# Kernel tuning notes

Hardware: AMD Instinct MI355X
Metric: run time of the kernel (lower is better)

The kernel has to match this reference:

```python
import jax, jax.numpy as jnp
import numpy as np
import math

B, T, C, H = 4, 2048, 1024, 4
D = C // H
SCALE = 1.0 / math.sqrt(D)
EPS = 1e-5

def _cln(x, w, b):
    # channel-first LayerNorm over C of (B, C, T)
    mu = jnp.mean(x, axis=1, keepdims=True)
    r = x - mu
    s = jnp.mean(r * r, axis=1, keepdims=True)
    return r / jnp.sqrt(s + EPS) * w + b

def _dwconv(x, w, b=None):
    # depthwise conv1d: x (B, C, T), w (C, 1, 3), stride 1, pad 1
    y = jax.lax.conv_general_dilated(x, w, (1,), [(1, 1)], dimension_numbers=('NCH', 'OIH', 'NCH'), feature_group_count=x.shape[1])
    if b is not None:
        y = y + b[None, :, None]
    return y

def _conv1x1(x, w, b):
    # pointwise conv: x (B, C, T), w (Cout, Cin), b (Cout,)
    return jnp.einsum('oc,bct->bot', w, x) + b[None, :, None]

def _forward(x, mask, norm1_w, norm1_b, qconv_w, kconv_w, vconv_w, qnorm_w, qnorm_b, knorm_w, knorm_b, vnorm_w, vnorm_b, q1_w, q1_b, k1_w, k1_b, v1_w, v1_b, proj_w, proj_b, norm2_w, norm2_b, lin1_w, lin1_b, tc_w, tc_b, lin2_w, lin2_b):
    xc = jnp.swapaxes(x, 1, 2)                      # (B, C, T)
    h = _cln(xc, norm1_w, norm1_b)
    mf = mask.astype(x.dtype)                       # (B, 1, T); stride 1 -> interpolate is identity
    q = _conv1x1(_cln(_dwconv(h, qconv_w) * mf, qnorm_w, qnorm_b), q1_w, q1_b)
    k = _conv1x1(_cln(_dwconv(h, kconv_w) * mf, knorm_w, knorm_b), k1_w, k1_b)
    v = _conv1x1(_cln(_dwconv(h, vconv_w) * mf, vnorm_w, vnorm_b), v1_w, v1_b)
    # (B, H, T, D)
    q = jnp.swapaxes(q.reshape(B, H, D, T), 2, 3)
    k = jnp.swapaxes(k.reshape(B, H, D, T), 2, 3)
    v = jnp.swapaxes(v.reshape(B, H, D, T), 2, 3)
    att = jnp.einsum('bhqd,bhkd->bhqk', q * SCALE, k)
    att = jnp.where(mask[:, :, None, :], att, -jnp.inf)
    att = jax.nn.softmax(att, axis=-1)
    out = jnp.einsum('bhqk,bhkd->bhqd', att, v * mf[:, :, :, None])
    out = jnp.swapaxes(out, 2, 3).reshape(B, C, T)
    out = _conv1x1(out, proj_w, proj_b) * mf        # qx_mask == mask for stride 1
    x = x + jnp.swapaxes(out, 1, 2)                 # residual, (B, T, C)
    # Local_cnn branch
    h2 = jnp.swapaxes(_cln(jnp.swapaxes(x, 1, 2), norm2_w, norm2_b), 1, 2)  # (B, T, C)
    y = h2 @ lin1_w.T + lin1_b
    y = jnp.swapaxes(_dwconv(jnp.swapaxes(y, 1, 2), tc_w, tc_b), 1, 2)
    y = jax.nn.gelu(y, approximate=False)
    y = y @ lin2_w.T + lin2_b
    return x + y

def setup_inputs():
    key = jax.random.key(0)
    ks = jax.random.split(key, 16)
    f32 = jnp.float32
    x = jax.random.normal(ks[0], (B, T, C), dtype=f32)
    lengths = jax.random.randint(ks[1], (B,), T // 2, T + 1)
    mask = jnp.arange(T)[None, None, :] < lengths[:, None, None]  # (B, 1, T) bool
    dw_std = math.sqrt(2.0 / 3.0)
    px_std = math.sqrt(2.0 / C)
    d = dict(x=x, mask=mask)
    d['norm1_w'] = jnp.ones((1, C, 1), f32); d['norm1_b'] = jnp.zeros((1, C, 1), f32)
    d['qconv_w'] = jax.random.normal(ks[2], (C, 1, 3), dtype=f32) * dw_std
    d['kconv_w'] = jax.random.normal(ks[3], (C, 1, 3), dtype=f32) * dw_std
    d['vconv_w'] = jax.random.normal(ks[4], (C, 1, 3), dtype=f32) * dw_std
    for nm in ['qnorm', 'knorm', 'vnorm']:
        d[nm + '_w'] = jnp.ones((1, C, 1), f32); d[nm + '_b'] = jnp.zeros((1, C, 1), f32)
    d['q1_w'] = jax.random.normal(ks[5], (C, C), dtype=f32) * px_std; d['q1_b'] = jnp.zeros((C,), f32)
    d['k1_w'] = jax.random.normal(ks[6], (C, C), dtype=f32) * px_std; d['k1_b'] = jnp.zeros((C,), f32)
    d['v1_w'] = jax.random.normal(ks[7], (C, C), dtype=f32) * px_std; d['v1_b'] = jnp.zeros((C,), f32)
    d['proj_w'] = jax.random.normal(ks[8], (C, C), dtype=f32) * px_std; d['proj_b'] = jnp.zeros((C,), f32)
    d['norm2_w'] = jnp.ones((1, C, 1), f32); d['norm2_b'] = jnp.zeros((1, C, 1), f32)
    d['lin1_w'] = jax.random.normal(ks[9], (C, C), dtype=f32) * 0.02; d['lin1_b'] = jnp.zeros((C,), f32)
    d['tc_w'] = jax.random.normal(ks[10], (C, 1, 3), dtype=f32) * dw_std; d['tc_b'] = jnp.zeros((C,), f32)
    d['lin2_w'] = jax.random.normal(ks[11], (C, C), dtype=f32) * 0.02; d['lin2_b'] = jnp.zeros((C,), f32)
    return d

def reference(x, mask, norm1_w, norm1_b, qconv_w, kconv_w, vconv_w, qnorm_w, qnorm_b, knorm_w, knorm_b, vnorm_w, vnorm_b, q1_w, q1_b, k1_w, k1_b, v1_w, v1_b, proj_w, proj_b, norm2_w, norm2_b, lin1_w, lin1_b, tc_w, tc_b, lin2_w, lin2_b):
    return _forward(x, mask, norm1_w, norm1_b, qconv_w, kconv_w, vconv_w, qnorm_w, qnorm_b, knorm_w, knorm_b, vnorm_w, vnorm_b, q1_w, q1_b, k1_w, k1_b, v1_w, v1_b, proj_w, proj_b, norm2_w, norm2_b, lin1_w, lin1_b, tc_w, tc_b, lin2_w, lin2_b)
```

## Files before the change

kernel.cpp:

```cpp
#include <hip/hip_runtime.h>

#define BB 4
#define TT 2048
#define CC 1024
#define HH 4
#define DD 256
#define MM (BB*TT)

#define EPSV 1e-5f
#define NEGBIG (-1e30f)
#define SCALEV 0.0625f

typedef unsigned short u16;
typedef unsigned int   u32;
typedef __bf16 bf16x8 __attribute__((ext_vector_type(8)));
typedef float  f32x4  __attribute__((ext_vector_type(4)));
typedef float  f32x16 __attribute__((ext_vector_type(16)));

typedef u32 __attribute__((address_space(1))) gu32;
typedef u32 __attribute__((address_space(3))) lu32;

__device__ __forceinline__ u16 f2bf(float f){
  u32 u = __builtin_bit_cast(u32, f);
  u32 r = (u + 0x7fffu + ((u >> 16) & 1u)) >> 16;
  return (u16)r;
}
__device__ __forceinline__ float bf2f(u16 h){
  u32 u = ((u32)h) << 16;
  return __builtin_bit_cast(float, u);
}
__device__ __forceinline__ void gload_lds16(const u16* g, u16* l){
  __builtin_amdgcn_global_load_lds((const gu32*)g, (lu32*)l, 16, 0, 0);
}
__device__ __forceinline__ u32 cvtpk_bf16(float lo, float hi){
  u32 r;
  asm("v_cvt_pk_bf16_f32 %0, %1, %2" : "=v"(r) : "v"(lo), "v"(hi));
  return r;
}

__global__ __launch_bounds__(256) void conv_w_kernel(
    const float* __restrict__ w0, const float* __restrict__ w1, const float* __restrict__ w2,
    const float* __restrict__ w3, const float* __restrict__ w4, const float* __restrict__ w5,
    u16* __restrict__ o0, u16* __restrict__ o1, u16* __restrict__ o2,
    u16* __restrict__ o3, u16* __restrict__ o4, u16* __restrict__ o5){
  const int i = (blockIdx.x * 256 + threadIdx.x) * 4;
  const float* wsrc[6] = {w0,w1,w2,w3,w4,w5};
  u16* odst[6] = {o0,o1,o2,o3,o4,o5};
#pragma unroll
  for (int k = 0; k < 6; ++k){
    float4 v = *(const float4*)(wsrc[k] + i);
    ushort4 p; p.x=f2bf(v.x); p.y=f2bf(v.y); p.z=f2bf(v.z); p.w=f2bf(v.w);
    *(ushort4*)(odst[k] + i) = p;
  }
}

template<int OUTBF>
__global__ __launch_bounds__(256) void ln_rows(const float* __restrict__ x,
    const float* __restrict__ g, const float* __restrict__ be, void* __restrict__ out){
  const int row = blockIdx.x, tid = threadIdx.x;
  const float4 v = ((const float4*)(x + (size_t)row * CC))[tid];
  float s  = v.x + v.y + v.z + v.w;
  float ss = v.x*v.x + v.y*v.y + v.z*v.z + v.w*v.w;
  __shared__ float sb[8];
#pragma unroll
  for (int o = 1; o < 64; o <<= 1){ s += __shfl_xor(s, o); ss += __shfl_xor(ss, o); }
  const int wid = tid >> 6, lane = tid & 63;
  if (lane == 0){ sb[wid] = s; sb[4 + wid] = ss; }
  __syncthreads();
  s  = sb[0] + sb[1] + sb[2] + sb[3];
  ss = sb[4] + sb[5] + sb[6] + sb[7];
  const float mu = s * (1.0f / CC);
  const float rstd = rsqrtf(ss * (1.0f / CC) - mu * mu + EPSV);
  const float4 gg = ((const float4*)g)[tid];
  const float4 bb = ((const float4*)be)[tid];
  const float r0 = (v.x - mu) * rstd * gg.x + bb.x;
  const float r1 = (v.y - mu) * rstd * gg.y + bb.y;
  const float r2 = (v.z - mu) * rstd * gg.z + bb.z;
  const float r3 = (v.w - mu) * rstd * gg.w + bb.w;
  if (OUTBF){
    ushort4 p; p.x=f2bf(r0); p.y=f2bf(r1); p.z=f2bf(r2); p.w=f2bf(r3);
    *(ushort4*)((u16*)out + (size_t)row * CC + tid * 4) = p;
  } else {
    ((float4*)((float*)out + (size_t)row * CC))[tid] = make_float4(r0, r1, r2, r3);
  }
}

__global__ __launch_bounds__(256) void qkv_pre(const float* __restrict__ h,
    const int* __restrict__ mask,
    const float* __restrict__ qw, const float* __restrict__ kw, const float* __restrict__ vw,
    const float* __restrict__ qg, const float* __restrict__ qb2,
    const float* __restrict__ kg, const float* __restrict__ kb2,
    const float* __restrict__ vg, const float* __restrict__ vb2,
    u16* __restrict__ qn, u16* __restrict__ kn, u16* __restrict__ vn){
  const int row = blockIdx.x, tid = threadIdx.x;
  const int t = row & (TT - 1);
  const float mf = mask[row] ? 1.f : 0.f;
  const float4 z4 = make_float4(0.f, 0.f, 0.f, 0.f);
  const float4 x0 = ((const float4*)(h + (size_t)row * CC))[tid];
  const float4 xm = (t > 0)      ? ((const float4*)(h + (size_t)(row - 1) * CC))[tid] : z4;
  const float4 xp = (t < TT - 1) ? ((const float4*)(h + (size_t)(row + 1) * CC))[tid] : z4;
  const int c = tid * 4;
  const float am[4] = {xm.x, xm.y, xm.z, xm.w};
  const float a0[4] = {x0.x, x0.y, x0.z, x0.w};
  const float ap[4] = {xp.x, xp.y, xp.z, xp.w};
  float yq[4], yk[4], yv[4];
  float sq=0.f, ssq=0.f, sk=0.f, ssk=0.f, sv=0.f, ssv=0.f;
#pragma unroll
  for (int i = 0; i < 4; ++i){
    const float* qwp = qw + (c + i) * 3;
    const float* kwp = kw + (c + i) * 3;
    const float* vwp = vw + (c + i) * 3;
    const float q_ = (am[i]*qwp[0] + a0[i]*qwp[1] + ap[i]*qwp[2]) * mf;
    const float k_ = (am[i]*kwp[0] + a0[i]*kwp[1] + ap[i]*kwp[2]) * mf;
    const float v_ = (am[i]*vwp[0] + a0[i]*vwp[1] + ap[i]*vwp[2]) * mf;
    yq[i]=q_; yk[i]=k_; yv[i]=v_;
    sq+=q_; ssq+=q_*q_; sk+=k_; ssk+=k_*k_; sv+=v_; ssv+=v_*v_;
  }
  __shared__ float sb[24];
#pragma unroll
  for (int o = 1; o < 64; o <<= 1){
    sq += __shfl_xor(sq, o); ssq += __shfl_xor(ssq, o);
    sk += __shfl_xor(sk, o); ssk += __shfl_xor(ssk, o);
    sv += __shfl_xor(sv, o); ssv += __shfl_xor(ssv, o);
  }
  const int wid = tid >> 6, lane = tid & 63;
  if (lane == 0){
    sb[wid]=sq; sb[4+wid]=ssq; sb[8+wid]=sk; sb[12+wid]=ssk; sb[16+wid]=sv; sb[20+wid]=ssv;
  }
  __syncthreads();
  sq  = sb[0]+sb[1]+sb[2]+sb[3];    ssq = sb[4]+sb[5]+sb[6]+sb[7];
  sk  = sb[8]+sb[9]+sb[10]+sb[11];  ssk = sb[12]+sb[13]+sb[14]+sb[15];
  sv  = sb[16]+sb[17]+sb[18]+sb[19];ssv = sb[20]+sb[21]+sb[22]+sb[23];
  {
    const float mu = sq * (1.f/CC), rstd = rsqrtf(ssq*(1.f/CC) - mu*mu + EPSV);
    ushort4 p;
    p.x = f2bf((yq[0]-mu)*rstd*qg[c+0] + qb2[c+0]);
    p.y = f2bf((yq[1]-mu)*rstd*qg[c+1] + qb2[c+1]);
    p.z = f2bf((yq[2]-mu)*rstd*qg[c+2] + qb2[c+2]);
    p.w = f2bf((yq[3]-mu)*rstd*qg[c+3] + qb2[c+3]);
    *(ushort4*)(qn + (size_t)row * CC + c) = p;
  }
  {
    const float mu = sk * (1.f/CC), rstd = rsqrtf(ssk*(1.f/CC) - mu*mu + EPSV);
    ushort4 p;
    p.x = f2bf((yk[0]-mu)*rstd*kg[c+0] + kb2[c+0]);
    p.y = f2bf((yk[1]-mu)*rstd*kg[c+1] + kb2[c+1]);
    p.z = f2bf((yk[2]-mu)*rstd*kg[c+2] + kb2[c+2]);
    p.w = f2bf((yk[3]-mu)*rstd*kg[c+3] + kb2[c+3]);
    *(ushort4*)(kn + (size_t)row * CC + c) = p;
  }
  {
    const float mu = sv * (1.f/CC), rstd = rsqrtf(ssv*(1.f/CC) - mu*mu + EPSV);
    ushort4 p;
    p.x = f2bf((yv[0]-mu)*rstd*vg[c+0] + vb2[c+0]);
    p.y = f2bf((yv[1]-mu)*rstd*vg[c+1] + vb2[c+1]);
    p.z = f2bf((yv[2]-mu)*rstd*vg[c+2] + vb2[c+2]);
    p.w = f2bf((yv[3]-mu)*rstd*vg[c+3] + vb2[c+3]);
    *(ushort4*)(vn + (size_t)row * CC + c) = p;
  }
}

__device__ __forceinline__ void gemm_core(const u16* __restrict__ A, const u16* __restrict__ Bw,
    u16* As, u16* Bs, f32x4 acc[4][4], int bm, int bn, int tid){
  const int lane = tid & 63, wid = tid >> 6;
  const int wr = wid >> 1, wc = wid & 1;
  const int la = lane & 15, lg = lane >> 4;
  const int srow = tid >> 3;
  const int schunk = (tid & 7) ^ (srow & 7);
  const u16* gA = A  + (size_t)(bm * 128 + srow) * CC + schunk * 8;
  const u16* gB = Bw + (size_t)(bn * 128 + srow) * CC + schunk * 8;
  u16* dA = As + tid * 8;
  u16* dB = Bs + tid * 8;
  const int swz = (la & 7) << 4;
  for (int kt = 0; kt < CC / 64; ++kt){
#pragma unroll
    for (int i = 0; i < 4; ++i){
      gload_lds16(gA + (size_t)(i * 32) * CC + kt * 64, dA + i * 2048);
      gload_lds16(gB + (size_t)(i * 32) * CC + kt * 64, dB + i * 2048);
    }
    __syncthreads();
#pragma unroll
    for (int kk = 0; kk < 2; ++kk){
      bf16x8 af[4], bf[4];
      const int co = (kk * 64 + lg * 16) ^ swz;
#pragma unroll
      for (int mi = 0; mi < 4; ++mi)
        af[mi] = *(const bf16x8*)((const char*)As + (wr * 64 + mi * 16 + la) * 128 + co);
#pragma unroll
      for (int ni = 0; ni < 4; ++ni)
        bf[ni] = *(const bf16x8*)((const char*)Bs + (wc * 64 + ni * 16 + la) * 128 + co);
#pragma unroll
      for (int mi = 0; mi < 4; ++mi)
#pragma unroll
        for (int ni = 0; ni < 4; ++ni)
          acc[mi][ni] = __builtin_amdgcn_mfma_f32_16x16x32_bf16(af[mi], bf[ni], acc[mi][ni], 0, 0, 0);
    }
    __syncthreads();
  }
}

template<int MODE>
__global__ __launch_bounds__(256) void gemm_bt(
    const u16* __restrict__ A, const u16* __restrict__ Bw,
    const float* __restrict__ bias, void* __restrict__ out,
    const float* __restrict__ resid, const int* __restrict__ mask){
  __shared__ __align__(16) u16 As[128 * 64];
  __shared__ __align__(16) u16 Bs[128 * 64];
  const int tid = threadIdx.x, lane = tid & 63, wid = tid >> 6;
  const int wr = wid >> 1, wc = wid & 1;
  const int bm = blockIdx.x, bn = blockIdx.y;
  f32x4 acc[4][4];
#pragma unroll
  for (int i = 0; i < 4; ++i)
#pragma unroll
    for (int j = 0; j < 4; ++j) acc[i][j] = (f32x4){0.f, 0.f, 0.f, 0.f};
  gemm_core(A, Bw, As, Bs, acc, bm, bn, tid);
  const int la = lane & 15, lg = lane >> 4;
#pragma unroll
  for (int mi = 0; mi < 4; ++mi){
    const int mb = bm * 128 + wr * 64 + mi * 16 + lg * 4;
#pragma unroll
    for (int ni = 0; ni < 4; ++ni){
      const int n = bn * 128 + wc * 64 + ni * 16 + la;
      const float bz = bias[n];
      if (MODE == 0){
        u16* o = (u16*)out;
#pragma unroll
        for (int j = 0; j < 4; ++j) o[(size_t)(mb + j) * CC + n] = f2bf(acc[mi][ni][j] + bz);
      } else if (MODE == 1){
        float* o = (float*)out;
#pragma unroll
        for (int j = 0; j < 4; ++j){
          const int m = mb + j;
          const float mf = mask[m] ? 1.f : 0.f;
          o[(size_t)m * CC + n] = (acc[mi][ni][j] + bz) * mf + resid[(size_t)m * CC + n];
        }
      } else {
        float* o = (float*)out;
#pragma unroll
        for (int j = 0; j < 4; ++j){
          const int m = mb + j;
          o[(size_t)m * CC + n] = acc[mi][ni][j] + bz + resid[(size_t)m * CC + n];
        }
      }
    }
  }
}

__global__ __launch_bounds__(256) void gemm_qkv(
    const u16* __restrict__ qn, const u16* __restrict__ kn, const u16* __restrict__ vn,
    const u16* __restrict__ wq, const u16* __restrict__ wk, const u16* __restrict__ wv,
    const float* __restrict__ qb, const float* __restrict__ kb, const float* __restrict__ vb,
    u16* __restrict__ Qb, u16* __restrict__ Kb, u16* __restrict__ Vtb){
  __shared__ __align__(16) u16 As[128 * 64];
  __shared__ __align__(16) u16 Bs[128 * 64];
  const int z = blockIdx.z;
  const u16* A  = (z == 0) ? qn : (z == 1) ? kn : vn;
  const u16* Bw = (z == 0) ? wq : (z == 1) ? wk : wv;
  const float* bias = (z == 0) ? qb : (z == 1) ? kb : vb;
  const int tid = threadIdx.x, lane = tid & 63, wid = tid >> 6;
  const int wr = wid >> 1, wc = wid & 1;
  const int bm = blockIdx.x, bn = blockIdx.y;
  f32x4 acc[4][4];
#pragma unroll
  for (int i = 0; i < 4; ++i)
#pragma unroll
    for (int j = 0; j < 4; ++j) acc[i][j] = (f32x4){0.f, 0.f, 0.f, 0.f};
  gemm_core(A, Bw, As, Bs, acc, bm, bn, tid);
  const int la = lane & 15, lg = lane >> 4;
#pragma unroll
  for (int mi = 0; mi < 4; ++mi){
    const int mb = bm * 128 + wr * 64 + mi * 16 + lg * 4;
#pragma unroll
    for (int ni = 0; ni < 4; ++ni){
      const int n = bn * 128 + wc * 64 + ni * 16 + la;
      const float bz = bias[n];
      if (z < 2){
        u16* o = z ? Kb : Qb;
#pragma unroll
        for (int j = 0; j < 4; ++j) o[(size_t)(mb + j) * CC + n] = f2bf(acc[mi][ni][j] + bz);
      } else {
        const int bq = mb >> 11, tq = mb & (TT - 1);
        const int hq = n >> 8, dq = n & 255;
        ushort4 p;
        p.x = f2bf(acc[mi][ni][0] + bz); p.y = f2bf(acc[mi][ni][1] + bz);
        p.z = f2bf(acc[mi][ni][2] + bz); p.w = f2bf(acc[mi][ni][3] + bz);
        *(ushort4*)&Vtb[(size_t)((bq * HH + hq) * DD + dq) * TT + tq] = p;
      }
    }
  }
}

__global__ __launch_bounds__(256, 2) void flash_attn(
    const u16* __restrict__ Q, const u16* __restrict__ Kg,
    const u16* __restrict__ Vt, const int* __restrict__ mask,
    u16* __restrict__ Os0, u16* __restrict__ Os1, float2* __restrict__ stats){
  __shared__ __align__(16) u16 Ks[32 * 256];
  __shared__ __align__(16) u16 Vs[256 * 32];
  const int Dn = blockIdx.x;
  const int xcd = Dn & 7, rest = Dn >> 3;
  const int bh = xcd * 2 + (rest >> 5);
  const int sub = rest & 31;
  const int qt = sub >> 1, sp = sub & 1;
  const int b = bh >> 2, h2 = bh & 3;
  const int tid = threadIdx.x, lane = tid & 63, wid = tid >> 6;
  const int l31 = lane & 31, hi = lane >> 5;

  const int* mrow = mask + b * TT;
  int len = 1024;
  {
    unsigned long long bal = __ballot(mrow[1024 + lane * 16] != 0);
    int ones = __popcll(bal);
    if (ones > 0){
      int lo = 1024 + (ones - 1) * 16;
      unsigned long long bal2 = __ballot(mrow[lo + (lane & 15)] != 0);
      len = lo + __popcll(bal2 & 0xFFFFull);
    }
  }
  const int nkt = (len + 31) >> 5;
  const int hk = (nkt + 1) >> 1;
  const int t0 = sp ? hk : 0, t1 = sp ? nkt : hk;

  const int q0 = qt * 128 + wid * 32;
  bf16x8 qf[16];
  const u16* qrow = Q + (size_t)(b * TT + q0 + l31) * CC + h2 * DD + hi * 8;
#pragma unroll
  for (int kd = 0; kd < 16; ++kd) qf[kd] = *(const bf16x8*)(qrow + kd * 16);

  f32x16 acc[8];
#pragma unroll
  for (int i = 0; i < 8; ++i)
#pragma unroll
    for (int r = 0; r < 16; ++r) acc[i][r] = 0.f;
  float mrun = NEGBIG, lrun = 0.f;

  const int krow = tid >> 5;
  const int kc = (tid & 31) ^ (krow & 7);
  const u16* ksrc = Kg + (size_t)(b * TT + krow) * CC + h2 * DD + kc * 8;
  const int vc = (tid & 3) ^ ((tid >> 3) & 3);
  const u16* vsrcb = Vt + (size_t)(bh * DD + (tid >> 2)) * TT + vc * 8;

#define STAGE_K(KT) { _Pragma("unroll") \
  for (int i = 0; i < 4; ++i) \
    gload_lds16(ksrc + (size_t)((KT) * 32 + i * 8) * CC, Ks + i * 2048 + tid * 8); }
#define STAGE_V(KT) { _Pragma("unroll") \
  for (int i = 0; i < 4; ++i) \
    gload_lds16(vsrcb + (size_t)(i * 64) * TT + (KT) * 32, Vs + i * 2048 + tid * 8); }

  STAGE_K(t0); STAGE_V(t0);
  __syncthreads();

  const char* KsB = (const char*)Ks;
  const char* VsB = (const char*)Vs;
  const int swk = (l31 & 7) << 4;
  const int swv = ((l31 >> 1) & 3) << 4;
  const float sc2 = SCALEV * 1.44269504f;

  for (int kt = t0; kt < t1; ++kt){
    f32x16 s;
#pragma unroll
    for (int r = 0; r < 16; ++r) s[r] = 0.f;
#pragma unroll
    for (int kd = 0; kd < 16; ++kd){
      bf16x8 kf = *(const bf16x8*)(KsB + l31 * 512 + ((kd * 32 + hi * 16) ^ swk));
      s = __builtin_amdgcn_mfma_f32_32x32x16_bf16(kf, qf[kd], s, 0, 0, 0);
    }
    if (kt * 32 + 32 <= len){
      s *= sc2;
    } else {
#pragma unroll
      for (int r = 0; r < 16; ++r){
        const int k = kt * 32 + (r & 3) + 8 * (r >> 2) + 4 * hi;
        s[r] = (k < len) ? s[r] * sc2 : NEGBIG;
      }
    }
    float tm = s[0];
#pragma unroll
    for (int r = 1; r < 16; ++r) tm = fmaxf(tm, s[r]);
    tm = fmaxf(tm, __shfl_xor(tm, 32));
    if (!__all(tm <= mrun + 12.0f)){
      const float mn = fmaxf(mrun, tm);
      const float al = __builtin_exp2f(mrun - mn);
      mrun = mn; lrun *= al;
#pragma unroll
      for (int i = 0; i < 8; ++i) acc[i] *= al;
    }
    float p[16];
    float ts = 0.f;
#pragma unroll
    for (int r = 0; r < 16; ++r){ p[r] = __builtin_exp2f(s[r] - mrun); ts += p[r]; }
    ts += __shfl_xor(ts, 32);
    lrun += ts;
    u32 w0 = cvtpk_bf16(p[0],  p[1]),  w1 = cvtpk_bf16(p[2],  p[3]);
    u32 w2 = cvtpk_bf16(p[4],  p[5]),  w3 = cvtpk_bf16(p[6],  p[7]);
    u32 w4 = cvtpk_bf16(p[8],  p[9]),  w5 = cvtpk_bf16(p[10], p[11]);
    u32 w6 = cvtpk_bf16(p[12], p[13]), w7 = cvtpk_bf16(p[14], p[15]);
    asm("v_permlane32_swap_b32 %0, %1" : "+v"(w0), "+v"(w2));
    asm("v_permlane32_swap_b32 %0, %1" : "+v"(w1), "+v"(w3));
    asm("v_permlane32_swap_b32 %0, %1" : "+v"(w4), "+v"(w6));
    asm("v_permlane32_swap_b32 %0, %1" : "+v"(w5), "+v"(w7));
    u32 pb0u[4] = {w0, w1, w2, w3};
    u32 pb1u[4] = {w4, w5, w6, w7};
    bf16x8 pb0 = __builtin_bit_cast(bf16x8, *(uint4*)pb0u);
    bf16x8 pb1 = __builtin_bit_cast(bf16x8, *(uint4*)pb1u);
    __syncthreads();
    if (kt + 1 < t1) STAGE_K(kt + 1);
#pragma unroll
    for (int dt = 0; dt < 8; ++dt){
      const char* vr = VsB + (dt * 32 + l31) * 64;
      bf16x8 vf0 = *(const bf16x8*)(vr + ((hi * 16) ^ swv));
      acc[dt] = __builtin_amdgcn_mfma_f32_32x32x16_bf16(vf0, pb0, acc[dt], 0, 0, 0);
      bf16x8 vf1 = *(const bf16x8*)(vr + ((32 + hi * 16) ^ swv));
      acc[dt] = __builtin_amdgcn_mfma_f32_32x32x16_bf16(vf1, pb1, acc[dt], 0, 0, 0);
    }
    __syncthreads();
    if (kt + 1 < t1) STAGE_V(kt + 1);
  }
  u16* Os = sp ? Os1 : Os0;
  u16* orow = Os + (size_t)(b * TT + q0 + l31) * CC + h2 * DD + hi * 4;
#pragma unroll
  for (int dt = 0; dt < 8; ++dt)
#pragma unroll
    for (int rg = 0; rg < 4; ++rg){
      ushort4 pk;
      pk.x = f2bf(acc[dt][rg * 4 + 0]); pk.y = f2bf(acc[dt][rg * 4 + 1]);
      pk.z = f2bf(acc[dt][rg * 4 + 2]); pk.w = f2bf(acc[dt][rg * 4 + 3]);
      *(ushort4*)(orow + dt * 32 + rg * 8) = pk;
    }
  if (lane < 32)
    stats[(size_t)((sp * 16 + bh) << 11) + q0 + l31] = make_float2(mrun, lrun);
#undef STAGE_K
#undef STAGE_V
}

__global__ __launch_bounds__(256) void attn_combine(
    const u16* __restrict__ Os0, const u16* __restrict__ Os1,
    const float2* __restrict__ stats, u16* __restrict__ AO){
  const int row = blockIdx.x, tid = threadIdx.x;
  const int b = row >> 11, q = row & (TT - 1);
  const int h2 = tid >> 6;
  const int bh = b * HH + h2;
  const float2 sA = stats[(size_t)(bh << 11) + q];
  const float2 sB = stats[(size_t)((16 + bh) << 11) + q];
  const float m = fmaxf(sA.x, sB.x);
  const float eA = __builtin_exp2f(sA.x - m), eB = __builtin_exp2f(sB.x - m);
  const float l = sA.y * eA + sB.y * eB;
  const float fA = eA / l, fB = eB / l;
  const size_t off = (size_t)row * CC + tid * 4;
  const ushort4 a = *(const ushort4*)(Os0 + off);
  const ushort4 c = *(const ushort4*)(Os1 + off);
  ushort4 o;
  o.x = f2bf(bf2f(a.x) * fA + bf2f(c.x) * fB);
  o.y = f2bf(bf2f(a.y) * fA + bf2f(c.y) * fB);
  o.z = f2bf(bf2f(a.z) * fA + bf2f(c.z) * fB);
  o.w = f2bf(bf2f(a.w) * fA + bf2f(c.w) * fB);
  *(ushort4*)(AO + off) = o;
}

__global__ __launch_bounds__(256) void tc_gelu(const u16* __restrict__ y2,
    const float* __restrict__ w, const float* __restrict__ bias, u16* __restrict__ y3){
  const int row = blockIdx.x, tid = threadIdx.x;
  const int t = row & (TT - 1);
  const int c = tid * 4;
  ushort4 z4; z4.x = z4.y = z4.z = z4.w = 0;
  const ushort4 u0 = *(const ushort4*)(y2 + (size_t)row * CC + c);
  const ushort4 um = (t > 0)      ? *(const ushort4*)(y2 + (size_t)(row - 1) * CC + c) : z4;
  const ushort4 up = (t < TT - 1) ? *(const ushort4*)(y2 + (size_t)(row + 1) * CC + c) : z4;
  const float am[4] = {bf2f(um.x), bf2f(um.y), bf2f(um.z), bf2f(um.w)};
  const float a0[4] = {bf2f(u0.x), bf2f(u0.y), bf2f(u0.z), bf2f(u0.w)};
  const float ap[4] = {bf2f(up.x), bf2f(up.y), bf2f(up.z), bf2f(up.w)};
  u16 pv[4];
#pragma unroll
  for (int i = 0; i < 4; ++i){
    const float* wp = w + (c + i) * 3;
    const float yv = am[i] * wp[0] + a0[i] * wp[1] + ap[i] * wp[2] + bias[c + i];
    const float ge = 0.5f * yv * (1.f + erff(yv * 0.7071067811865475f));
    pv[i] = f2bf(ge);
  }
  ushort4 p; p.x = pv[0]; p.y = pv[1]; p.z = pv[2]; p.w = pv[3];
  *(ushort4*)(y3 + (size_t)row * CC + c) = p;
}

extern "C" void kernel_launch(void* const* d_in, const int* in_sizes, int n_in,
                              void* d_out, int out_size, void* d_ws, size_t ws_size,
                              hipStream_t stream){
  const float* x     = (const float*)d_in[0];
  const int*   mask  = (const int*)d_in[1];
  const float* n1g   = (const float*)d_in[2];
  const float* n1b   = (const float*)d_in[3];
  const float* qconv = (const float*)d_in[4];
  const float* kconv = (const float*)d_in[5];
  const float* vconv = (const float*)d_in[6];
  const float* qg    = (const float*)d_in[7];
  const float* qbe   = (const float*)d_in[8];
  const float* kg    = (const float*)d_in[9];
  const float* kbe   = (const float*)d_in[10];
  const float* vg    = (const float*)d_in[11];
  const float* vbe   = (const float*)d_in[12];
  const float* q1w   = (const float*)d_in[13];
  const float* q1b   = (const float*)d_in[14];
  const float* k1w   = (const float*)d_in[15];
  const float* k1b   = (const float*)d_in[16];
  const float* v1w   = (const float*)d_in[17];
  const float* v1b   = (const float*)d_in[18];
  const float* pw    = (const float*)d_in[19];
  const float* pb    = (const float*)d_in[20];
  const float* n2g   = (const float*)d_in[21];
  const float* n2b   = (const float*)d_in[22];
  const float* l1w   = (const float*)d_in[23];
  const float* l1b   = (const float*)d_in[24];
  const float* tcw   = (const float*)d_in[25];
  const float* tcb   = (const float*)d_in[26];
  const float* l2w   = (const float*)d_in[27];
  const float* l2b   = (const float*)d_in[28];
  (void)in_sizes; (void)n_in; (void)out_size; (void)ws_size;

  char* ws = (char*)d_ws;
  const size_t MB = (size_t)1 << 20;
  u16* wq  = (u16*)(ws + 0 * MB);
  u16* wk  = (u16*)(ws + 2 * MB);
  u16* wv  = (u16*)(ws + 4 * MB);
  u16* wp2 = (u16*)(ws + 6 * MB);
  u16* wl1 = (u16*)(ws + 8 * MB);
  u16* wl2 = (u16*)(ws + 10 * MB);
  float* hbuf = (float*)(ws + 12 * MB);
  float* x2   = hbuf;
  u16* qn  = (u16*)(ws + 44 * MB);
  u16* kn  = (u16*)(ws + 60 * MB);
  u16* vn  = (u16*)(ws + 76 * MB);
  u16* Qb  = (u16*)(ws + 92 * MB);
  u16* Kb  = (u16*)(ws + 108 * MB);
  u16* Vtb = (u16*)(ws + 124 * MB);
  float2* stats = (float2*)(ws + 140 * MB);
  u16* AO  = qn;
  u16* Os0 = kn;
  u16* Os1 = vn;
  u16* y1  = kn;
  u16* y2  = vn;
  u16* y3  = Qb;

  conv_w_kernel<<<1024, 256, 0, stream>>>(q1w, k1w, v1w, pw, l1w, l2w, wq, wk, wv, wp2, wl1, wl2);
  ln_rows<0><<<MM, 256, 0, stream>>>(x, n1g, n1b, hbuf);
  qkv_pre<<<MM, 256, 0, stream>>>(hbuf, mask, qconv, kconv, vconv,
                                  qg, qbe, kg, kbe, vg, vbe, qn, kn, vn);
  gemm_qkv<<<dim3(64, 8, 3), 256, 0, stream>>>(qn, kn, vn, wq, wk, wv, q1b, k1b, v1b, Qb, Kb, Vtb);
  flash_attn<<<512, 256, 0, stream>>>(Qb, Kb, Vtb, mask, Os0, Os1, stats);
  attn_combine<<<MM, 256, 0, stream>>>(Os0, Os1, stats, AO);
  gemm_bt<1><<<dim3(64, 8), 256, 0, stream>>>(AO, wp2, pb, x2, x, mask);
  ln_rows<1><<<MM, 256, 0, stream>>>(x2, n2g, n2b, y1);
  gemm_bt<0><<<dim3(64, 8), 256, 0, stream>>>(y1, wl1, l1b, y2, nullptr, nullptr);
  tc_gelu<<<MM, 256, 0, stream>>>(y2, tcw, tcb, y3);
  gemm_bt<2><<<dim3(64, 8), 256, 0, stream>>>(y3, wl2, l2b, (float*)d_out, x2, nullptr);
}
```

Baseline: 340.4 us.

## Store LN1 output in bf16, halve flash-attn block size, raise GEMM occupancy hints

The first LayerNorm now writes bf16 instead of fp32, so the depthwise-conv/QKV pre-kernel reads half the bytes. Flash attention moves from 256-thread blocks covering 128 queries to 128-thread blocks covering 64 queries, doubling the grid to 1024 blocks, with K/V staging loops and index remapping adjusted to match. The GEMM kernels gain a min-blocks-per-CU hint of 3 to push more waves per CU, at the risk of register spills. The bf16 LN output adds rounding error ahead of the conv and norm stages.

```diff
diff --git a/kernel.cpp b/kernel.cpp
--- a/kernel.cpp
+++ b/kernel.cpp
@@ -85,7 +85,7 @@
   }
 }
 
-__global__ __launch_bounds__(256) void qkv_pre(const float* __restrict__ h,
+__global__ __launch_bounds__(256) void qkv_pre(const u16* __restrict__ h,
     const int* __restrict__ mask,
     const float* __restrict__ qw, const float* __restrict__ kw, const float* __restrict__ vw,
     const float* __restrict__ qg, const float* __restrict__ qb2,
@@ -95,14 +95,14 @@
   const int row = blockIdx.x, tid = threadIdx.x;
   const int t = row & (TT - 1);
   const float mf = mask[row] ? 1.f : 0.f;
-  const float4 z4 = make_float4(0.f, 0.f, 0.f, 0.f);
-  const float4 x0 = ((const float4*)(h + (size_t)row * CC))[tid];
-  const float4 xm = (t > 0)      ? ((const float4*)(h + (size_t)(row - 1) * CC))[tid] : z4;
-  const float4 xp = (t < TT - 1) ? ((const float4*)(h + (size_t)(row + 1) * CC))[tid] : z4;
+  ushort4 z4; z4.x = z4.y = z4.z = z4.w = 0;
+  const ushort4 x0 = ((const ushort4*)(h + (size_t)row * CC))[tid];
+  const ushort4 xm = (t > 0)      ? ((const ushort4*)(h + (size_t)(row - 1) * CC))[tid] : z4;
+  const ushort4 xp = (t < TT - 1) ? ((const ushort4*)(h + (size_t)(row + 1) * CC))[tid] : z4;
   const int c = tid * 4;
-  const float am[4] = {xm.x, xm.y, xm.z, xm.w};
-  const float a0[4] = {x0.x, x0.y, x0.z, x0.w};
-  const float ap[4] = {xp.x, xp.y, xp.z, xp.w};
+  const float am[4] = {bf2f(xm.x), bf2f(xm.y), bf2f(xm.z), bf2f(xm.w)};
+  const float a0[4] = {bf2f(x0.x), bf2f(x0.y), bf2f(x0.z), bf2f(x0.w)};
+  const float ap[4] = {bf2f(xp.x), bf2f(xp.y), bf2f(xp.z), bf2f(xp.w)};
   float yq[4], yk[4], yv[4];
   float sq=0.f, ssq=0.f, sk=0.f, ssk=0.f, sv=0.f, ssv=0.f;
 #pragma unroll
@@ -200,7 +200,7 @@
 }
 
 template<int MODE>
-__global__ __launch_bounds__(256) void gemm_bt(
+__global__ __launch_bounds__(256, 3) void gemm_bt(
     const u16* __restrict__ A, const u16* __restrict__ Bw,
     const float* __restrict__ bias, void* __restrict__ out,
     const float* __restrict__ resid, const int* __restrict__ mask){
@@ -247,7 +247,7 @@
   }
 }
 
-__global__ __launch_bounds__(256) void gemm_qkv(
+__global__ __launch_bounds__(256, 3) void gemm_qkv(
     const u16* __restrict__ qn, const u16* __restrict__ kn, const u16* __restrict__ vn,
     const u16* __restrict__ wq, const u16* __restrict__ wk, const u16* __restrict__ wv,
     const float* __restrict__ qb, const float* __restrict__ kb, const float* __restrict__ vb,
@@ -291,7 +291,7 @@
   }
 }
 
-__global__ __launch_bounds__(256, 2) void flash_attn(
+__global__ __launch_bounds__(128, 2) void flash_attn(
     const u16* __restrict__ Q, const u16* __restrict__ Kg,
     const u16* __restrict__ Vt, const int* __restrict__ mask,
     u16* __restrict__ Os0, u16* __restrict__ Os1, float2* __restrict__ stats){
@@ -299,8 +299,8 @@
   __shared__ __align__(16) u16 Vs[256 * 32];
   const int Dn = blockIdx.x;
   const int xcd = Dn & 7, rest = Dn >> 3;
-  const int bh = xcd * 2 + (rest >> 5);
-  const int sub = rest & 31;
+  const int bh = xcd * 2 + (rest >> 6);
+  const int sub = rest & 63;
   const int qt = sub >> 1, sp = sub & 1;
   const int b = bh >> 2, h2 = bh & 3;
   const int tid = threadIdx.x, lane = tid & 63, wid = tid >> 6;
@@ -321,7 +321,7 @@
   const int hk = (nkt + 1) >> 1;
   const int t0 = sp ? hk : 0, t1 = sp ? nkt : hk;
 
-  const int q0 = qt * 128 + wid * 32;
+  const int q0 = qt * 64 + wid * 32;
   bf16x8 qf[16];
   const u16* qrow = Q + (size_t)(b * TT + q0 + l31) * CC + h2 * DD + hi * 8;
 #pragma unroll
@@ -334,18 +334,18 @@
     for (int r = 0; r < 16; ++r) acc[i][r] = 0.f;
   float mrun = NEGBIG, lrun = 0.f;
 
-  const int krow = tid >> 5;
-  const int kc = (tid & 31) ^ (krow & 7);
-  const u16* ksrc = Kg + (size_t)(b * TT + krow) * CC + h2 * DD + kc * 8;
-  const int vc = (tid & 3) ^ ((tid >> 3) & 3);
-  const u16* vsrcb = Vt + (size_t)(bh * DD + (tid >> 2)) * TT + vc * 8;
+  const int kr0 = tid >> 5;
+  const u16* ksrcE = Kg + (size_t)(b * TT + kr0) * CC + h2 * DD + (((tid & 31) ^ kr0) * 8);
+  const u16* ksrcO = Kg + (size_t)(b * TT + kr0) * CC + h2 * DD + (((tid & 31) ^ (kr0 | 4)) * 8);
+  const u16* vsrc  = Vt + (size_t)(bh * DD + (tid >> 2)) * TT + (((tid & 3) ^ ((tid >> 3) & 3)) * 8);
 
 #define STAGE_K(KT) { _Pragma("unroll") \
-  for (int i = 0; i < 4; ++i) \
-    gload_lds16(ksrc + (size_t)((KT) * 32 + i * 8) * CC, Ks + i * 2048 + tid * 8); }
+  for (int i = 0; i < 8; ++i){ \
+    const u16* srcp = (i & 1) ? ksrcO : ksrcE; \
+    gload_lds16(srcp + (size_t)((KT) * 32 + i * 4) * CC, Ks + i * 1024 + tid * 8); } }
 #define STAGE_V(KT) { _Pragma("unroll") \
-  for (int i = 0; i < 4; ++i) \
-    gload_lds16(vsrcb + (size_t)(i * 64) * TT + (KT) * 32, Vs + i * 2048 + tid * 8); }
+  for (int i = 0; i < 8; ++i) \
+    gload_lds16(vsrc + (size_t)(i * 32) * TT + (KT) * 32, Vs + i * 1024 + tid * 8); }
 
   STAGE_K(t0); STAGE_V(t0);
   __syncthreads();
@@ -427,7 +427,7 @@
       pk.z = f2bf(acc[dt][rg * 4 + 2]); pk.w = f2bf(acc[dt][rg * 4 + 3]);
       *(ushort4*)(orow + dt * 32 + rg * 8) = pk;
     }
-  if (lane < 32)
+  if ((lane & 32) == 0)
     stats[(size_t)((sp * 16 + bh) << 11) + q0 + l31] = make_float2(mrun, lrun);
 #undef STAGE_K
 #undef STAGE_V
@@ -523,8 +523,8 @@
   u16* wp2 = (u16*)(ws + 6 * MB);
   u16* wl1 = (u16*)(ws + 8 * MB);
   u16* wl2 = (u16*)(ws + 10 * MB);
-  float* hbuf = (float*)(ws + 12 * MB);
-  float* x2   = hbuf;
+  u16* hbuf = (u16*)(ws + 12 * MB);
+  float* x2 = (float*)(ws + 12 * MB);
   u16* qn  = (u16*)(ws + 44 * MB);
   u16* kn  = (u16*)(ws + 60 * MB);
   u16* vn  = (u16*)(ws + 76 * MB);
@@ -540,11 +540,11 @@
   u16* y3  = Qb;
 
   conv_w_kernel<<<1024, 256, 0, stream>>>(q1w, k1w, v1w, pw, l1w, l2w, wq, wk, wv, wp2, wl1, wl2);
-  ln_rows<0><<<MM, 256, 0, stream>>>(x, n1g, n1b, hbuf);
+  ln_rows<1><<<MM, 256, 0, stream>>>(x, n1g, n1b, hbuf);
   qkv_pre<<<MM, 256, 0, stream>>>(hbuf, mask, qconv, kconv, vconv,
                                   qg, qbe, kg, kbe, vg, vbe, qn, kn, vn);
   gemm_qkv<<<dim3(64, 8, 3), 256, 0, stream>>>(qn, kn, vn, wq, wk, wv, q1b, k1b, v1b, Qb, Kb, Vtb);
-  flash_attn<<<512, 256, 0, stream>>>(Qb, Kb, Vtb, mask, Os0, Os1, stats);
+  flash_attn<<<1024, 128, 0, stream>>>(Qb, Kb, Vtb, mask, Os0, Os1, stats);
   attn_combine<<<MM, 256, 0, stream>>>(Os0, Os1, stats, AO);
   gemm_bt<1><<<dim3(64, 8), 256, 0, stream>>>(AO, wp2, pb, x2, x, mask);
   ln_rows<1><<<MM, 256, 0, stream>>>(x2, n2g, n2b, y1);
```

Result: no change. 345.5 us (+1.5%).
